# Kernel tuning notes

Hardware: AMD Instinct MI355X
Metric: run time of the kernel (lower is better)

The kernel has to match this reference:

```python
import jax, jax.numpy as jnp
import numpy as np

NUM_NODES = 64   # EEG channels / input size
D = 512          # rnn1 hidden size
N_LAYERS = 3
B, T = 32, 1024


def _lstm_dir(x, W_ih, W_hh, b_ih, b_hh, reverse=False):
    """Single-direction LSTM layer (torch gate order i,f,g,o).
    x: [B,T,I], W_ih: [4H,I], W_hh: [4H,H], biases: [4H]. Returns [B,T,H]."""
    H = W_hh.shape[1]
    # Precompute input projection for all timesteps (big GEMM, compute-bound).
    xp = jnp.einsum('bti,gi->btg', x, W_ih) + (b_ih + b_hh)  # [B,T,4H]

    def step(carry, xt):
        h, c = carry
        gates = xt + h @ W_hh.T                 # [B,4H]
        i, f, g, o = jnp.split(gates, 4, axis=-1)
        i = jax.nn.sigmoid(i)
        f = jax.nn.sigmoid(f)
        g = jnp.tanh(g)
        o = jax.nn.sigmoid(o)
        c = f * c + i * g
        h = o * jnp.tanh(c)
        return (h, c), h

    init = (jnp.zeros((x.shape[0], H), x.dtype), jnp.zeros((x.shape[0], H), x.dtype))
    _, hs = jax.lax.scan(step, init, jnp.swapaxes(xp, 0, 1), reverse=reverse)
    return jnp.swapaxes(hs, 0, 1)  # [B,T,H]


def _bilstm(x, W_ih, W_hh, b_ih, b_hh):
    """Bidirectional layer; params stacked on leading dir axis [2,...]."""
    fwd = _lstm_dir(x, W_ih[0], W_hh[0], b_ih[0], b_hh[0], reverse=False)
    bwd = _lstm_dir(x, W_ih[1], W_hh[1], b_ih[1], b_hh[1], reverse=True)
    return jnp.concatenate([fwd, bwd], axis=-1)  # [B,T,2H]


def setup_inputs() -> dict:
    key = jax.random.key(0)
    ks = jax.random.split(key, 16)
    k1 = 1.0 / np.sqrt(D)          # torch LSTM init bound for rnn1
    k2 = 1.0 / np.sqrt(NUM_NODES)  # for rnn2
    u = lambda k, shape, b: jax.random.uniform(k, shape, jnp.float32, -b, b)
    inp = {
        'x': jax.random.normal(ks[0], (B, T, NUM_NODES), jnp.float32),
        # rnn1 layer 0: input NUM_NODES, 2 directions
        'W_ih_l0': u(ks[1], (2, 4 * D, NUM_NODES), k1),
        'W_hh_l0': u(ks[2], (2, 4 * D, D), k1),
        'b_ih_l0': u(ks[3], (2, 4 * D), k1),
        'b_hh_l0': u(ks[4], (2, 4 * D), k1),
        # rnn1 layers 1-2: input 2*D, stacked [layer, dir, ...]
        'W_ih_l12': u(ks[5], (2, 2, 4 * D, 2 * D), k1),
        'W_hh_l12': u(ks[6], (2, 2, 4 * D, D), k1),
        'b_ih_l12': u(ks[7], (2, 2, 4 * D), k1),
        'b_hh_l12': u(ks[8], (2, 2, 4 * D), k1),
        # rnn2: single unidirectional layer, input 2*D, hidden NUM_NODES
        'W_ih2': u(ks[9], (4 * NUM_NODES, 2 * D), k2),
        'W_hh2': u(ks[10], (4 * NUM_NODES, NUM_NODES), k2),
        'b_ih2': u(ks[11], (4 * NUM_NODES,), k2),
        'b_hh2': u(ks[12], (4 * NUM_NODES,), k2),
    }
    return inp


def reference(x, W_ih_l0, W_hh_l0, b_ih_l0, b_hh_l0,
              W_ih_l12, W_hh_l12, b_ih_l12, b_hh_l12,
              W_ih2, W_hh2, b_ih2, b_hh2):
    out = _bilstm(x, W_ih_l0, W_hh_l0, b_ih_l0, b_hh_l0)        # [B,T,2D]
    for l in range(N_LAYERS - 1):
        out = _bilstm(out, W_ih_l12[l], W_hh_l12[l], b_ih_l12[l], b_hh_l12[l])
    out = _lstm_dir(out, W_ih2, W_hh2, b_ih2, b_hh2)            # [B,T,NUM_NODES]
    return out * 40.0
```

## Files before the change

### kernel.cpp

```cpp
#include <hip/hip_runtime.h>
#include <stdio.h>
#include <stdint.h>

#define BB 32
#define TT 1024
#define DH 512
#define ND 64
#define TC 128

typedef short bf16x8 __attribute__((ext_vector_type(8)));
typedef float f32x4  __attribute__((ext_vector_type(4)));

static __device__ __forceinline__ float bf2f(unsigned short u) {
    union { unsigned int i; float f; } v; v.i = ((unsigned int)u) << 16; return v.f;
}
static __device__ __forceinline__ unsigned short f2bf_rne(float f) {
    union { float f; unsigned int i; } v; v.f = f;
    unsigned int u = v.i;
    return (unsigned short)((u + 0x7fffu + ((u >> 16) & 1u)) >> 16);
}
static __device__ __forceinline__ float sigm(float x) { return 1.f / (1.f + __expf(-x)); }
static __device__ __forceinline__ float tanhs(float x) {
    float ax = fabsf(x);
    float e = __expf(-2.f * ax);
    float t = (1.f - e) / (1.f + e);
    return x < 0.f ? -t : t;
}

__global__ void k_f2bf(const float* __restrict__ src, unsigned short* __restrict__ dst, int n4) {
    int i = blockIdx.x * blockDim.x + threadIdx.x;
    if (i < n4) {
        float4 v = ((const float4*)src)[i];
        ushort4 o;
        o.x = f2bf_rne(v.x); o.y = f2bf_rne(v.y); o.z = f2bf_rne(v.z); o.w = f2bf_rne(v.w);
        ((ushort4*)dst)[i] = o;
    }
}

__global__ void k_bsum(const float* __restrict__ a, const float* __restrict__ b,
                       float* __restrict__ d, int n) {
    int i = blockIdx.x * blockDim.x + threadIdx.x;
    if (i < n) d[i] = a[i] + b[i];
}

__global__ __launch_bounds__(256) void k_gemm(
    const unsigned short* __restrict__ A,
    const unsigned short* __restrict__ W,
    const float* __restrict__ bias,
    unsigned short* __restrict__ out,
    int N, int K)
{
    __shared__ unsigned short lw[128 * 72];
    __shared__ unsigned short la[128 * 72];
    const int tid = threadIdx.x;
    const int n0 = blockIdx.x * 128;
    const int m0 = blockIdx.y * 128;
    const int lane = tid & 63, wv = tid >> 6;
    const int q = lane >> 4, lr = lane & 15;
    const int wn = wv & 1, wm = wv >> 1;

    f32x4 acc[4][4];
#pragma unroll
    for (int i = 0; i < 4; i++)
#pragma unroll
        for (int j = 0; j < 4; j++) acc[i][j] = (f32x4){0.f, 0.f, 0.f, 0.f};

    const int srow = tid >> 1, shalf = tid & 1;
    for (int k0 = 0; k0 < K; k0 += 64) {
        const uint4* gw = (const uint4*)(W + (size_t)(n0 + srow) * K + k0 + shalf * 32);
        const uint4* ga = (const uint4*)(A + (size_t)(m0 + srow) * K + k0 + shalf * 32);
        uint4 wld[4], ald[4];
#pragma unroll
        for (int j = 0; j < 4; j++) { wld[j] = gw[j]; ald[j] = ga[j]; }
        __syncthreads();
#pragma unroll
        for (int j = 0; j < 4; j++) {
            ((uint4*)lw)[srow * 9 + shalf * 4 + j] = wld[j];
            ((uint4*)la)[srow * 9 + shalf * 4 + j] = ald[j];
        }
        __syncthreads();
#pragma unroll
        for (int ks = 0; ks < 2; ks++) {
            bf16x8 fw[4], fa[4];
#pragma unroll
            for (int i = 0; i < 4; i++)
                fw[i] = *(const bf16x8*)&lw[(64 * wn + 16 * i + lr) * 72 + ks * 32 + q * 8];
#pragma unroll
            for (int j = 0; j < 4; j++)
                fa[j] = *(const bf16x8*)&la[(64 * wm + 16 * j + lr) * 72 + ks * 32 + q * 8];
#pragma unroll
            for (int i = 0; i < 4; i++)
#pragma unroll
                for (int j = 0; j < 4; j++)
                    acc[i][j] = __builtin_amdgcn_mfma_f32_16x16x32_bf16(fw[i], fa[j], acc[i][j], 0, 0, 0);
        }
    }
#pragma unroll
    for (int i = 0; i < 4; i++) {
        const int nb = n0 + 64 * wn + 16 * i + q * 4;
        const float4 bb = *(const float4*)(bias + nb);
#pragma unroll
        for (int j = 0; j < 4; j++) {
            const int m = m0 + 64 * wm + 16 * j + lr;
            const int rowp = ((m & 1023) << 5) | (m >> 10);
            ushort4 o;
            o.x = f2bf_rne(acc[i][j][0] + bb.x);
            o.y = f2bf_rne(acc[i][j][1] + bb.y);
            o.z = f2bf_rne(acc[i][j][2] + bb.z);
            o.w = f2bf_rne(acc[i][j][3] + bb.w);
            *(ushort4*)(out + (size_t)rowp * N + nb) = o;
        }
    }
}

__global__ __launch_bounds__(512) void k_layer(
    const unsigned short* A,
    const unsigned short* wih,
    const float* bias,
    const unsigned short* whh,
    unsigned short* __restrict__ outb,
    unsigned short* xpc,
    unsigned short* hbuf,
    unsigned int* ctl, int K)
{
    extern __shared__ unsigned short smem[];
    const int tid = threadIdx.x;
    const int bid = blockIdx.x;
    unsigned int* chunkready = ctl;
    unsigned int* rnnprog = ctl + 128;
    unsigned int* stepflag = ctl + 256;

    if (bid < 64) {
        unsigned short* lw = smem;
        unsigned short* lh = smem + 128 * 520;
        float* lg = (float*)(smem + 128 * 520 + 16 * 520);
        const int dir = bid & 1;
        const int bg = (bid >> 1) & 1;
        const int cs = bid >> 2;
        const int c0 = cs * 32, b0 = bg * 16;
        const int lane = tid & 63, wv = tid >> 6;
        const int q = lane >> 4, lr = lane & 15;

        for (int i = tid; i < 128 * 64; i += 512) {
            int row = i >> 6, ch = i & 63;
            int ty = row >> 5, cc = row & 31;
            ((uint4*)lw)[row * 65 + ch] =
                *(const uint4*)(whh + ((size_t)(dir * 2048 + ty * 512 + c0 + cc) * 512 + ch * 8));
        }
        const int xb = tid >> 5;
        const int xc = tid & 31;
        float cstate = 0.f;
        unsigned int* myflag = stepflag + ((dir * 2 + bg) * 16 + cs) * 16;
        const unsigned int* grpflag = stepflag + (dir * 2 + bg) * 256;
        __syncthreads();

        for (int s = 0; s < TT; ++s) {
            if ((s & (TC - 1)) == 0) {
                const int c = s >> 7;
                if (tid == 0) {
                    while (__hip_atomic_load(&chunkready[c * 16], __ATOMIC_RELAXED,
                                             __HIP_MEMORY_SCOPE_AGENT) < 128u)
                        __builtin_amdgcn_s_sleep(8);
                }
                __syncthreads();
                __builtin_amdgcn_fence(__ATOMIC_ACQUIRE, "agent");
            }
            const unsigned short* xpb = xpc + (size_t)((s >> 7) & 1) * (TC * 32ull * 4096);
            const int t = dir ? (TT - 1 - s) : s;
            const unsigned short* xpp = xpb + ((size_t)((s & (TC - 1)) * 32 + b0 + xb) * 4096)
                                       + dir * 2048 + c0 + xc;
            unsigned short x0 = xpp[0], x1 = xpp[512], x2 = xpp[1024], x3 = xpp[1536];

            if (s > 0) {
                const int pp = (s & 1) ^ 1;
                const unsigned short* hb = hbuf + ((size_t)(dir * 2 + pp) * 32 + b0) * 512;
#pragma unroll
                for (int i = tid; i < 16 * 128; i += 512) {
                    int row = i >> 7, ch = i & 127;
                    unsigned long long v = __hip_atomic_load(
                        (const unsigned long long*)(hb + row * 512 + ch * 4),
                        __ATOMIC_RELAXED, __HIP_MEMORY_SCOPE_AGENT);
                    *(unsigned long long*)&((unsigned int*)lh)[row * 260 + ch * 2] = v;
                }
                __syncthreads();
                f32x4 acc = (f32x4){0.f, 0.f, 0.f, 0.f};
                const unsigned short* lwr = lw + (16 * wv + lr) * 520;
                const unsigned short* lhr = lh + lr * 520;
#pragma unroll
                for (int ks = 0; ks < 16; ++ks) {
                    bf16x8 a = *(const bf16x8*)(lwr + ks * 32 + q * 8);
                    bf16x8 b = *(const bf16x8*)(lhr + ks * 32 + q * 8);
                    acc = __builtin_amdgcn_mfma_f32_16x16x32_bf16(a, b, acc, 0, 0, 0);
                }
#pragma unroll
                for (int r = 0; r < 4; ++r)
                    lg[(16 * wv + q * 4 + r) * 17 + lr] = acc[r];
                __syncthreads();
            }

            {
                float gi = bf2f(x0) + (s > 0 ? lg[(0 * 32 + xc) * 17 + xb] : 0.f);
                float gf = bf2f(x1) + (s > 0 ? lg[(1 * 32 + xc) * 17 + xb] : 0.f);
                float gg = bf2f(x2) + (s > 0 ? lg[(2 * 32 + xc) * 17 + xb] : 0.f);
                float go = bf2f(x3) + (s > 0 ? lg[(3 * 32 + xc) * 17 + xb] : 0.f);
                float ig = sigm(gi), fg = sigm(gf), cg = tanhs(gg), og = sigm(go);
                cstate = fg * cstate + ig * cg;
                float h = og * tanhs(cstate);
                unsigned short h16 = f2bf_rne(h);
                unsigned int hv = h16;
                unsigned int other = __shfl_xor((int)hv, 1);
                if ((tid & 1) == 0) {
                    size_t idx = ((size_t)(dir * 2 + (s & 1)) * 32 + b0 + xb) * 512 + c0 + xc;
                    unsigned int packed = hv | (other << 16);
                    __hip_atomic_store((unsigned int*)hbuf + (idx >> 1), packed,
                                       __ATOMIC_RELAXED, __HIP_MEMORY_SCOPE_AGENT);
                }
                outb[((size_t)(b0 + xb) * TT + t) * 1024 + dir * 512 + c0 + xc] = h16;
            }

            __syncthreads();
            if (tid == 0)
                __hip_atomic_store(myflag, (unsigned int)(s + 1),
                                   __ATOMIC_RELAXED, __HIP_MEMORY_SCOPE_AGENT);
            if (wv == 0) {
                const unsigned int tgt = (unsigned int)(s + 1);
                const unsigned int* fl = grpflag + (lane & 15) * 16;
                for (;;) {
                    unsigned int v = (lane < 16)
                        ? __hip_atomic_load(fl, __ATOMIC_RELAXED, __HIP_MEMORY_SCOPE_AGENT)
                        : tgt;
                    if (__all((int)(v >= tgt))) break;
                    __builtin_amdgcn_s_sleep(1);
                }
            }
            __syncthreads();
            if ((s & (TC - 1)) == (TC - 1) && tid == 0)
                __hip_atomic_fetch_add(rnnprog, 1u, __ATOMIC_RELAXED, __HIP_MEMORY_SCOPE_AGENT);
        }
    } else {
        const int w = bid - 64;
        const int engine = tid >> 8;
        const int etid = tid & 255;
        unsigned short* lw = smem + engine * 18432;
        unsigned short* la = lw + 9216;
        const int lane = etid & 63, wv = etid >> 6;
        const int q = lane >> 4, lr = lane & 15;
        const int wn = wv & 1, wm = wv >> 1;
        const int srow = etid >> 1, shalf = etid & 1;

        for (int c = 0; c < 8; ++c) {
            if (c >= 2) {
                if (tid == 0) {
                    unsigned int tgt = 64u * (unsigned int)(c - 1);
                    while (__hip_atomic_load(rnnprog, __ATOMIC_RELAXED,
                                             __HIP_MEMORY_SCOPE_AGENT) < tgt)
                        __builtin_amdgcn_s_sleep(8);
                }
                __syncthreads();
            }
            unsigned short* xpb = xpc + (size_t)(c & 1) * (TC * 32ull * 4096);
            for (int jt = 0; jt < 4; ++jt) {
                const int tau = (w * 2 + engine) + 256 * jt;
                const int dir = tau >> 9, rem = tau & 511;
                const int b = rem >> 4, nx = rem & 15;
                const int t0 = dir ? (TT - c * TC - TC) : (c * TC);
                const int n0 = dir * 2048 + nx * 128;
                const int m0 = b * TT + t0;
                f32x4 acc[4][4];
#pragma unroll
                for (int i = 0; i < 4; i++)
#pragma unroll
                    for (int j = 0; j < 4; j++) acc[i][j] = (f32x4){0.f, 0.f, 0.f, 0.f};

                for (int k0 = 0; k0 < K; k0 += 64) {
                    const uint4* gw = (const uint4*)(wih + (size_t)(n0 + srow) * K + k0 + shalf * 32);
                    const uint4* ga = (const uint4*)(A + (size_t)(m0 + srow) * K + k0 + shalf * 32);
                    uint4 wld[4], ald[4];
#pragma unroll
                    for (int j = 0; j < 4; j++) { wld[j] = gw[j]; ald[j] = ga[j]; }
                    __syncthreads();
#pragma unroll
                    for (int j = 0; j < 4; j++) {
                        ((uint4*)lw)[srow * 9 + shalf * 4 + j] = wld[j];
                        ((uint4*)la)[srow * 9 + shalf * 4 + j] = ald[j];
                    }
                    __syncthreads();
#pragma unroll
                    for (int ks = 0; ks < 2; ks++) {
                        bf16x8 fw[4], fa[4];
#pragma unroll
                        for (int i = 0; i < 4; i++)
                            fw[i] = *(const bf16x8*)&lw[(64 * wn + 16 * i + lr) * 72 + ks * 32 + q * 8];
#pragma unroll
                        for (int j = 0; j < 4; j++)
                            fa[j] = *(const bf16x8*)&la[(64 * wm + 16 * j + lr) * 72 + ks * 32 + q * 8];
#pragma unroll
                        for (int i = 0; i < 4; i++)
#pragma unroll
                            for (int j = 0; j < 4; j++)
                                acc[i][j] = __builtin_amdgcn_mfma_f32_16x16x32_bf16(fw[i], fa[j], acc[i][j], 0, 0, 0);
                    }
                }
#pragma unroll
                for (int i = 0; i < 4; i++) {
                    const int nb = n0 + 64 * wn + 16 * i + q * 4;
                    const float4 bb = *(const float4*)(bias + nb);
#pragma unroll
                    for (int j = 0; j < 4; j++) {
                        const int dm = 64 * wm + 16 * j + lr;
                        const int islot = dir ? (TC - 1 - dm) : dm;
                        ushort4 o;
                        o.x = f2bf_rne(acc[i][j][0] + bb.x);
                        o.y = f2bf_rne(acc[i][j][1] + bb.y);
                        o.z = f2bf_rne(acc[i][j][2] + bb.z);
                        o.w = f2bf_rne(acc[i][j][3] + bb.w);
                        *(ushort4*)(xpb + ((size_t)islot * 32 + b) * 4096 + nb) = o;
                    }
                }
            }
            __builtin_amdgcn_fence(__ATOMIC_RELEASE, "agent");
            __syncthreads();
            if (tid == 0)
                __hip_atomic_fetch_add(&chunkready[c * 16], 1u,
                                       __ATOMIC_RELEASE, __HIP_MEMORY_SCOPE_AGENT);
        }
    }
}

__global__ __launch_bounds__(512) void k_rnn2(
    const unsigned short* __restrict__ xp2,
    const unsigned short* __restrict__ whh2,
    float* __restrict__ out)
{
    __shared__ unsigned short lw[256 * 72];
    __shared__ unsigned short lh[2][16 * 68];
    const int tid = threadIdx.x;
    const int b0 = blockIdx.x * 16;
    const int lane = tid & 63, wv = tid >> 6;
    const int q = lane >> 4, l = lane & 15;

    for (int i = tid; i < 256 * 8; i += 512) {
        int row = i >> 3, ch = i & 7;
        ((uint4*)lw)[row * 9 + ch] = *(const uint4*)(whh2 + (size_t)row * 64 + ch * 8);
    }
    __syncthreads();

    if (wv < 4) {
        const int cbase = wv * 16 + q * 4;
        float cst[4] = {0.f, 0.f, 0.f, 0.f};
        for (int s = 0; s < TT; ++s) {
            const unsigned short* xr = xp2 + (size_t)(s * 32 + b0 + l) * 256 + cbase;
            ushort4 xv0 = *(const ushort4*)(xr);
            ushort4 xv1 = *(const ushort4*)(xr + 64);
            ushort4 xv2 = *(const ushort4*)(xr + 128);
            ushort4 xv3 = *(const ushort4*)(xr + 192);
            f32x4 acc[4];
            if (s > 0) {
                const unsigned short* lhr = lh[(s & 1) ^ 1] + l * 68;
                bf16x8 hb0 = *(const bf16x8*)(lhr + q * 8);
                bf16x8 hb1 = *(const bf16x8*)(lhr + 32 + q * 8);
#pragma unroll
                for (int ty = 0; ty < 4; ++ty) {
                    const unsigned short* lwr = lw + (size_t)(ty * 64 + wv * 16 + l) * 72;
                    bf16x8 a0 = *(const bf16x8*)(lwr + q * 8);
                    bf16x8 a1 = *(const bf16x8*)(lwr + 32 + q * 8);
                    f32x4 tacc = (f32x4){0.f, 0.f, 0.f, 0.f};
                    tacc = __builtin_amdgcn_mfma_f32_16x16x32_bf16(a0, hb0, tacc, 0, 0, 0);
                    tacc = __builtin_amdgcn_mfma_f32_16x16x32_bf16(a1, hb1, tacc, 0, 0, 0);
                    acc[ty] = tacc;
                }
            } else {
#pragma unroll
                for (int ty = 0; ty < 4; ++ty) acc[ty] = (f32x4){0.f, 0.f, 0.f, 0.f};
            }
            ushort4 ho; float4 oo;
            const unsigned short* xs0 = (const unsigned short*)&xv0;
            const unsigned short* xs1 = (const unsigned short*)&xv1;
            const unsigned short* xs2 = (const unsigned short*)&xv2;
            const unsigned short* xs3 = (const unsigned short*)&xv3;
#pragma unroll
            for (int r = 0; r < 4; ++r) {
                float gi = bf2f(xs0[r]) + acc[0][r];
                float gf = bf2f(xs1[r]) + acc[1][r];
                float gg = bf2f(xs2[r]) + acc[2][r];
                float go = bf2f(xs3[r]) + acc[3][r];
                float ig = sigm(gi), fg = sigm(gf), cg = tanhs(gg), og = sigm(go);
                cst[r] = fg * cst[r] + ig * cg;
                float h = og * tanhs(cst[r]);
                ((float*)&oo)[r] = 40.f * h;
                ((unsigned short*)&ho)[r] = f2bf_rne(h);
            }
            *(ushort4*)(lh[s & 1] + l * 68 + cbase) = ho;
            *(float4*)(out + ((size_t)(b0 + l) * TT + s) * 64 + cbase) = oo;
            __syncthreads();
        }
    } else {
        for (int s = 0; s < TT; ++s) __syncthreads();
    }
}

extern "C" void kernel_launch(void* const* d_in, const int* in_sizes, int n_in,
                              void* d_out, int out_size, void* d_ws, size_t ws_size,
                              hipStream_t stream) {
    (void)in_sizes; (void)n_in; (void)out_size;
    const float* x     = (const float*)d_in[0];
    const float* Wih0  = (const float*)d_in[1];
    const float* Whh0  = (const float*)d_in[2];
    const float* bih0  = (const float*)d_in[3];
    const float* bhh0  = (const float*)d_in[4];
    const float* Wih12 = (const float*)d_in[5];
    const float* Whh12 = (const float*)d_in[6];
    const float* bih12 = (const float*)d_in[7];
    const float* bhh12 = (const float*)d_in[8];
    const float* Wih2  = (const float*)d_in[9];
    const float* Whh2  = (const float*)d_in[10];
    const float* bih2  = (const float*)d_in[11];
    const float* bhh2  = (const float*)d_in[12];
    float* out = (float*)d_out;

    char* ws = (char*)d_ws;
    size_t off = 0;
    auto alloc = [&](size_t sz) { char* p = ws + off; off += (sz + 255) & ~(size_t)255; return p; };
    unsigned short* actA  = (unsigned short*)alloc(33554432ull * 2);
    unsigned short* actB  = (unsigned short*)alloc(33554432ull * 2);
    unsigned short* xpc   = (unsigned short*)alloc(2ull * TC * 32 * 4096 * 2);
    unsigned short* xbf   = (unsigned short*)alloc(2097152ull * 2);
    unsigned short* wihc  = (unsigned short*)alloc(4194304ull * 2);
    unsigned short* whhc  = (unsigned short*)alloc(2097152ull * 2);
    unsigned short* wih2b = (unsigned short*)alloc(262144ull * 2);
    unsigned short* whh2b = (unsigned short*)alloc(16384ull * 2);
    float* bs  = (float*)alloc(4096 * 4);
    float* bs2 = (float*)alloc(256 * 4);
    unsigned short* hbuf = (unsigned short*)alloc(2ull * 2 * 32 * 512 * 2);
    unsigned int* ctrl = (unsigned int*)alloc(8192);

    if (ws_size < off) {
        fprintf(stderr, "[kernel_launch] ws_size=%zu < needed=%zu — aborting cleanly\n", ws_size, off);
        return;
    }

    auto cvt = [&](const float* s, unsigned short* d, int n) {
        int n4 = n / 4;
        k_f2bf<<<(n4 + 255) / 256, 256, 0, stream>>>(s, d, n4);
    };
    cvt(x, xbf, 2097152);
    cvt(Wih2, wih2b, 262144);
    cvt(Whh2, whh2b, 16384);
    k_bsum<<<1, 256, 0, stream>>>(bih2, bhh2, bs2, 256);

    hipError_t rc = hipFuncSetAttribute(reinterpret_cast<const void*>(k_layer),
                                        hipFuncAttributeMaxDynamicSharedMemorySize, 160 * 1024);
    if (rc != hipSuccess) fprintf(stderr, "[kernel_launch] hipFuncSetAttribute rc=%d\n", (int)rc);
    const size_t layer_lds = (size_t)(128 * 520 + 16 * 520) * 2 + (size_t)128 * 17 * 4;

    for (int l = 0; l < 3; ++l) {
        const unsigned short* Abuf;
        unsigned short* Obuf;
        int K;
        if (l == 0) {
            cvt(Wih0, wihc, 262144);
            cvt(Whh0, whhc, 2097152);
            k_bsum<<<16, 256, 0, stream>>>(bih0, bhh0, bs, 4096);
            Abuf = xbf; Obuf = actA; K = 64;
        } else {
            cvt(Wih12 + (size_t)(l - 1) * 4194304, wihc, 4194304);
            cvt(Whh12 + (size_t)(l - 1) * 2097152, whhc, 2097152);
            k_bsum<<<16, 256, 0, stream>>>(bih12 + (l - 1) * 4096, bhh12 + (l - 1) * 4096, bs, 4096);
            Abuf = (l == 1) ? actA : actB;
            Obuf = (l == 1) ? actB : actA;
            K = 1024;
        }
        hipMemsetAsync(ctrl, 0, 8192, stream);
        k_layer<<<192, 512, layer_lds, stream>>>(Abuf, wihc, bs, whhc, Obuf, xpc, hbuf, ctrl, K);
    }

    k_gemm<<<dim3(2, 256), 256, 0, stream>>>(actA, wih2b, bs2, xpc, 256, 1024);
    k_rnn2<<<2, 512, 0, stream>>>(xpc, whh2b, out);
}
```

Measured before the change: 13.93 ms.

## Interleave both LSTM directions in each recurrent block to hide barrier latency

Each of the 64 recurrent blocks now owns 16 hidden columns for both the forward and backward directions instead of 32 columns of one direction. It alternates the two directions every step, so the cross-block flag wait for one direction overlaps with the other direction's work. The K=512 reduction is split across two wave halves and summed when the gates are read. The wait spin drops its sleep, and the flag array is widened to 32 blocks per group. In exchange, half the threads sit idle during the gate update and each step now carries more barriers.

```diff
diff --git a/kernel.cpp b/kernel.cpp
--- a/kernel.cpp
+++ b/kernel.cpp
@@ -134,24 +134,25 @@
         unsigned short* lw = smem;
         unsigned short* lh = smem + 128 * 520;
         float* lg = (float*)(smem + 128 * 520 + 16 * 520);
-        const int dir = bid & 1;
-        const int bg = (bid >> 1) & 1;
-        const int cs = bid >> 2;
-        const int c0 = cs * 32, b0 = bg * 16;
+        const int bg = bid & 1;
+        const int cs = bid >> 1;
+        const int c0 = cs * 16, b0 = bg * 16;
         const int lane = tid & 63, wv = tid >> 6;
         const int q = lane >> 4, lr = lane & 15;
+        const int ty = wv & 3, kh = wv >> 2;
 
         for (int i = tid; i < 128 * 64; i += 512) {
             int row = i >> 6, ch = i & 63;
-            int ty = row >> 5, cc = row & 31;
+            int d = row >> 6, rr = row & 63;
+            int t2 = rr >> 4, cc = rr & 15;
             ((uint4*)lw)[row * 65 + ch] =
-                *(const uint4*)(whh + ((size_t)(dir * 2048 + ty * 512 + c0 + cc) * 512 + ch * 8));
-        }
-        const int xb = tid >> 5;
-        const int xc = tid & 31;
-        float cstate = 0.f;
-        unsigned int* myflag = stepflag + ((dir * 2 + bg) * 16 + cs) * 16;
-        const unsigned int* grpflag = stepflag + (dir * 2 + bg) * 256;
+                *(const uint4*)(whh + ((size_t)(d * 2048 + t2 * 512 + c0 + cc) * 512 + ch * 8));
+        }
+        const int xb = (tid >> 4) & 15;
+        const int xc = tid & 15;
+        float cst[2] = {0.f, 0.f};
+        unsigned int* flagF = stepflag + ((0 * 2 + bg) * 32 + cs) * 16;
+        unsigned int* flagB = stepflag + ((1 * 2 + bg) * 32 + cs) * 16;
         __syncthreads();
 
         for (int s = 0; s < TT; ++s) {
@@ -166,74 +167,89 @@
                 __builtin_amdgcn_fence(__ATOMIC_ACQUIRE, "agent");
             }
             const unsigned short* xpb = xpc + (size_t)((s >> 7) & 1) * (TC * 32ull * 4096);
-            const int t = dir ? (TT - 1 - s) : s;
-            const unsigned short* xpp = xpb + ((size_t)((s & (TC - 1)) * 32 + b0 + xb) * 4096)
-                                       + dir * 2048 + c0 + xc;
-            unsigned short x0 = xpp[0], x1 = xpp[512], x2 = xpp[1024], x3 = xpp[1536];
-
-            if (s > 0) {
-                const int pp = (s & 1) ^ 1;
-                const unsigned short* hb = hbuf + ((size_t)(dir * 2 + pp) * 32 + b0) * 512;
-#pragma unroll
-                for (int i = tid; i < 16 * 128; i += 512) {
-                    int row = i >> 7, ch = i & 127;
-                    unsigned long long v = __hip_atomic_load(
-                        (const unsigned long long*)(hb + row * 512 + ch * 4),
-                        __ATOMIC_RELAXED, __HIP_MEMORY_SCOPE_AGENT);
-                    *(unsigned long long*)&((unsigned int*)lh)[row * 260 + ch * 2] = v;
+            const int slot = s & (TC - 1);
+            unsigned short xv[2][4];
+            if (tid < 256) {
+#pragma unroll
+                for (int d = 0; d < 2; ++d) {
+                    const unsigned short* xpp = xpb + ((size_t)(slot * 32 + b0 + xb) * 4096)
+                                               + d * 2048 + c0 + xc;
+                    xv[d][0] = xpp[0]; xv[d][1] = xpp[512]; xv[d][2] = xpp[1024]; xv[d][3] = xpp[1536];
+                }
+            }
+
+#pragma unroll
+            for (int d = 0; d < 2; ++d) {
+                const int t = d ? (TT - 1 - s) : s;
+                unsigned int* myflag = d ? flagB : flagF;
+                if (s > 0) {
+                    if (wv == 0) {
+                        const unsigned int tgt = (unsigned int)s;
+                        const unsigned int* fl = stepflag + ((d * 2 + bg) * 32 + (lane & 31)) * 16;
+                        for (;;) {
+                            unsigned int v = (lane < 32)
+                                ? __hip_atomic_load(fl, __ATOMIC_RELAXED, __HIP_MEMORY_SCOPE_AGENT)
+                                : tgt;
+                            if (__all((int)(v >= tgt))) break;
+                        }
+                    }
+                    __syncthreads();
+                    const int pp = (s & 1) ^ 1;
+                    const unsigned short* hb = hbuf + ((size_t)(d * 2 + pp) * 32 + b0) * 512;
+#pragma unroll
+                    for (int i = tid; i < 16 * 128; i += 512) {
+                        int row = i >> 7, ch = i & 127;
+                        unsigned long long v = __hip_atomic_load(
+                            (const unsigned long long*)(hb + row * 512 + ch * 4),
+                            __ATOMIC_RELAXED, __HIP_MEMORY_SCOPE_AGENT);
+                        *(unsigned long long*)&((unsigned int*)lh)[row * 260 + ch * 2] = v;
+                    }
+                    __syncthreads();
+                    f32x4 acc = (f32x4){0.f, 0.f, 0.f, 0.f};
+                    const unsigned short* lwr = lw + (size_t)(d * 64 + ty * 16 + lr) * 520 + kh * 256;
+                    const unsigned short* lhr = lh + (size_t)lr * 520 + kh * 256;
+#pragma unroll
+                    for (int ks = 0; ks < 8; ++ks) {
+                        bf16x8 a = *(const bf16x8*)(lwr + ks * 32 + q * 8);
+                        bf16x8 b = *(const bf16x8*)(lhr + ks * 32 + q * 8);
+                        acc = __builtin_amdgcn_mfma_f32_16x16x32_bf16(a, b, acc, 0, 0, 0);
+                    }
+#pragma unroll
+                    for (int r = 0; r < 4; ++r)
+                        lg[(size_t)(kh * 64 + ty * 16 + q * 4 + r) * 17 + lr] = acc[r];
+                    __syncthreads();
+                }
+
+                unsigned short h16 = 0;
+                if (tid < 256) {
+                    float gi = bf2f(xv[d][0]), gf = bf2f(xv[d][1]);
+                    float gg = bf2f(xv[d][2]), go = bf2f(xv[d][3]);
+                    if (s > 0) {
+                        gi += lg[(size_t)(0 * 16 + xc) * 17 + xb] + lg[(size_t)(64 + 0 * 16 + xc) * 17 + xb];
+                        gf += lg[(size_t)(1 * 16 + xc) * 17 + xb] + lg[(size_t)(64 + 1 * 16 + xc) * 17 + xb];
+                        gg += lg[(size_t)(2 * 16 + xc) * 17 + xb] + lg[(size_t)(64 + 2 * 16 + xc) * 17 + xb];
+                        go += lg[(size_t)(3 * 16 + xc) * 17 + xb] + lg[(size_t)(64 + 3 * 16 + xc) * 17 + xb];
+                    }
+                    float ig = sigm(gi), fg = sigm(gf), cg = tanhs(gg), og = sigm(go);
+                    cst[d] = fg * cst[d] + ig * cg;
+                    float h = og * tanhs(cst[d]);
+                    h16 = f2bf_rne(h);
+                    unsigned int hv = h16;
+                    unsigned int other = __shfl_xor((int)hv, 1);
+                    if ((tid & 1) == 0) {
+                        size_t idx = ((size_t)(d * 2 + (s & 1)) * 32 + b0 + xb) * 512 + c0 + xc;
+                        unsigned int packed = hv | (other << 16);
+                        __hip_atomic_store((unsigned int*)hbuf + (idx >> 1), packed,
+                                           __ATOMIC_RELAXED, __HIP_MEMORY_SCOPE_AGENT);
+                    }
                 }
                 __syncthreads();
-                f32x4 acc = (f32x4){0.f, 0.f, 0.f, 0.f};
-                const unsigned short* lwr = lw + (16 * wv + lr) * 520;
-                const unsigned short* lhr = lh + lr * 520;
-#pragma unroll
-                for (int ks = 0; ks < 16; ++ks) {
-                    bf16x8 a = *(const bf16x8*)(lwr + ks * 32 + q * 8);
-                    bf16x8 b = *(const bf16x8*)(lhr + ks * 32 + q * 8);
-                    acc = __builtin_amdgcn_mfma_f32_16x16x32_bf16(a, b, acc, 0, 0, 0);
-                }
-#pragma unroll
-                for (int r = 0; r < 4; ++r)
-                    lg[(16 * wv + q * 4 + r) * 17 + lr] = acc[r];
-                __syncthreads();
-            }
-
-            {
-                float gi = bf2f(x0) + (s > 0 ? lg[(0 * 32 + xc) * 17 + xb] : 0.f);
-                float gf = bf2f(x1) + (s > 0 ? lg[(1 * 32 + xc) * 17 + xb] : 0.f);
-                float gg = bf2f(x2) + (s > 0 ? lg[(2 * 32 + xc) * 17 + xb] : 0.f);
-                float go = bf2f(x3) + (s > 0 ? lg[(3 * 32 + xc) * 17 + xb] : 0.f);
-                float ig = sigm(gi), fg = sigm(gf), cg = tanhs(gg), og = sigm(go);
-                cstate = fg * cstate + ig * cg;
-                float h = og * tanhs(cstate);
-                unsigned short h16 = f2bf_rne(h);
-                unsigned int hv = h16;
-                unsigned int other = __shfl_xor((int)hv, 1);
-                if ((tid & 1) == 0) {
-                    size_t idx = ((size_t)(dir * 2 + (s & 1)) * 32 + b0 + xb) * 512 + c0 + xc;
-                    unsigned int packed = hv | (other << 16);
-                    __hip_atomic_store((unsigned int*)hbuf + (idx >> 1), packed,
+                if (tid == 0)
+                    __hip_atomic_store(myflag, (unsigned int)(s + 1),
                                        __ATOMIC_RELAXED, __HIP_MEMORY_SCOPE_AGENT);
-                }
-                outb[((size_t)(b0 + xb) * TT + t) * 1024 + dir * 512 + c0 + xc] = h16;
-            }
-
-            __syncthreads();
-            if (tid == 0)
-                __hip_atomic_store(myflag, (unsigned int)(s + 1),
-                                   __ATOMIC_RELAXED, __HIP_MEMORY_SCOPE_AGENT);
-            if (wv == 0) {
-                const unsigned int tgt = (unsigned int)(s + 1);
-                const unsigned int* fl = grpflag + (lane & 15) * 16;
-                for (;;) {
-                    unsigned int v = (lane < 16)
-                        ? __hip_atomic_load(fl, __ATOMIC_RELAXED, __HIP_MEMORY_SCOPE_AGENT)
-                        : tgt;
-                    if (__all((int)(v >= tgt))) break;
-                    __builtin_amdgcn_s_sleep(1);
-                }
-            }
-            __syncthreads();
+                if (tid < 256)
+                    outb[((size_t)(b0 + xb) * TT + t) * 1024 + d * 512 + c0 + xc] = h16;
+            }
             if ((s & (TC - 1)) == (TC - 1) && tid == 0)
                 __hip_atomic_fetch_add(rnnprog, 1u, __ATOMIC_RELAXED, __HIP_MEMORY_SCOPE_AGENT);
         }
@@ -432,7 +448,7 @@
     float* bs  = (float*)alloc(4096 * 4);
     float* bs2 = (float*)alloc(256 * 4);
     unsigned short* hbuf = (unsigned short*)alloc(2ull * 2 * 32 * 512 * 2);
-    unsigned int* ctrl = (unsigned int*)alloc(8192);
+    unsigned int* ctrl = (unsigned int*)alloc(16384);
 
     if (ws_size < off) {
         fprintf(stderr, "[kernel_launch] ws_size=%zu < needed=%zu — aborting cleanly\n", ws_size, off);
@@ -470,7 +486,7 @@
             Obuf = (l == 1) ? actB : actA;
             K = 1024;
         }
-        hipMemsetAsync(ctrl, 0, 8192, stream);
+        hipMemsetAsync(ctrl, 0, 16384, stream);
         k_layer<<<192, 512, layer_lds, stream>>>(Abuf, wihc, bs, whhc, Obuf, xpc, hbuf, ctrl, K);
     }
 
```

Result: slower. 19.94 ms (+43.2%).
